# Performance work log

Measured on AMD Instinct MI355X. Metric: run time of the kernel, lower is better.

The kernel has to match this reference:

```python
import jax, jax.numpy as jnp
import numpy as np
from jax import lax


def setup_inputs() -> dict:
    key = jax.random.key(0)
    ks = jax.random.split(key, 5)
    T, H, F, E = 2048, 1024, 2816, 8
    scale_h = 1.0 / np.sqrt(H)
    scale_f = 1.0 / np.sqrt(F)
    return {
        "x": jax.random.normal(ks[0], (T, H), dtype=jnp.float32),
        "router_w": jax.random.normal(ks[1], (H, E), dtype=jnp.float32) * scale_h,
        "w_gate": jax.random.normal(ks[2], (E, H, F), dtype=jnp.float32) * scale_h,
        "w_up": jax.random.normal(ks[3], (E, H, F), dtype=jnp.float32) * scale_h,
        "w_down": jax.random.normal(ks[4], (E, F, H), dtype=jnp.float32) * scale_f,
        "top_k": 2,
    }


def reference(x, router_w, w_gate, w_up, w_down, top_k):
    # x: [T, H] flat tokens; router_w: [H, E]; experts: SwiGLU FFN (silu(x Wg) * (x Wu)) Wd
    T = x.shape[0]
    E = router_w.shape[1]
    logits = x @ router_w                              # [T, E]
    probs = jax.nn.softmax(logits, axis=-1)            # router_use_softmax
    top_v, top_i = lax.top_k(probs, top_k)             # [T, K]
    top_v = top_v / jnp.sum(top_v, axis=-1, keepdims=True)  # normalize_topk_prob
    # dense combine weights [T, E], zero outside top-k (top-k indices are unique per row)
    comb = jnp.zeros((T, E), dtype=x.dtype).at[jnp.arange(T)[:, None], top_i].set(top_v)

    def expert_step(acc, args):
        wg, wu, wd, c = args                           # wg/wu: [H,F], wd: [F,H], c: [T]
        g = jnp.einsum("th,hf->tf", x, wg)
        u = jnp.einsum("th,hf->tf", x, wu)
        y = jnp.einsum("tf,fh->th", jax.nn.silu(g) * u, wd)
        return acc + c[:, None] * y, None

    out, _ = lax.scan(expert_step, jnp.zeros_like(x), (w_gate, w_up, w_down, comb.T))
    return out
```

## Files before the change

kernel.cpp:

```cpp
#include <hip/hip_runtime.h>
#include <hip/hip_bf16.h>
#include <cstdint>
#include <cstddef>

#define TT 2048
#define HH 1024
#define FF 2816
#define EE 8
#define BK 64
#define KT1 (HH / BK)
#define KT2 (FF / BK)
#define KS 4
#define KTPER (KT2 / KS)
#define NROWS (TT * 2)

typedef short bf16x8 __attribute__((ext_vector_type(8)));
typedef float f32x4v __attribute__((ext_vector_type(4)));
typedef float vf4    __attribute__((ext_vector_type(4)));
typedef unsigned int uint32;

typedef __attribute__((address_space(3))) unsigned int lds_u32;
typedef const __attribute__((address_space(1))) unsigned int glb_u32;

__device__ __forceinline__ void gll16(const void* g, unsigned char* l) {
    __builtin_amdgcn_global_load_lds((glb_u32*)g, (lds_u32*)l, 16, 0, 0);
}

__device__ __forceinline__ unsigned short f2bf(float f) {
    union { float f; uint32 u; } v; v.f = f;
    uint32 u = v.u;
    uint32 r = (u + 0x7FFFu + ((u >> 16) & 1u)) >> 16;
    return (unsigned short)r;
}

__device__ __forceinline__ void seg_of(const int* __restrict__ counts, int e,
                                       int& seg0, int& n_e) {
    int s = 0;
#pragma unroll
    for (int i = 0; i < EE; ++i) s += (i < e) ? counts[i] : 0;
    seg0 = s; n_e = counts[e];
}

__global__ void k_router(const float* __restrict__ x, const float* __restrict__ rw,
                         unsigned short* __restrict__ xb,
                         int* __restrict__ tke, float* __restrict__ tkw,
                         int* __restrict__ counts)
{
    int t = blockIdx.x * 4 + (threadIdx.x >> 6);
    int lane = threadIdx.x & 63;
    const float* xr = x + (size_t)t * HH;
    unsigned short* xbr = xb + (size_t)t * HH;
    float acc[EE];
#pragma unroll
    for (int e = 0; e < EE; ++e) acc[e] = 0.f;
#pragma unroll
    for (int i = 0; i < HH / 64; ++i) {
        int h = i * 64 + lane;
        float xv = xr[h];
        xbr[h] = f2bf(xv);
        const vf4* w = (const vf4*)(rw + (size_t)h * EE);
        vf4 w0 = w[0], w1 = w[1];
#pragma unroll
        for (int e = 0; e < 4; ++e) {
            acc[e]     = fmaf(xv, w0[e], acc[e]);
            acc[4 + e] = fmaf(xv, w1[e], acc[4 + e]);
        }
    }
#pragma unroll
    for (int e = 0; e < EE; ++e) {
        float v = acc[e];
#pragma unroll
        for (int m = 1; m < 64; m <<= 1) v += __shfl_xor(v, m, 64);
        acc[e] = v;
    }
    if (lane == 0) {
        int e1 = 0; float l1 = acc[0];
#pragma unroll
        for (int e = 1; e < EE; ++e) if (acc[e] > l1) { l1 = acc[e]; e1 = e; }
        int e2 = (e1 == 0) ? 1 : 0; float l2 = acc[e2];
#pragma unroll
        for (int e = 0; e < EE; ++e) if (e != e1 && acc[e] > l2) { l2 = acc[e]; e2 = e; }
        float w1 = 1.f / (1.f + __expf(l2 - l1));
        float w2 = 1.f - w1;
        tke[t * 2] = e1; tke[t * 2 + 1] = e2;
        tkw[t * 2] = w1; tkw[t * 2 + 1] = w2;
        atomicAdd(&counts[e1], 1);
        atomicAdd(&counts[e2], 1);
    }
}

__global__ __launch_bounds__(256)
void k_convert_w2(const float* __restrict__ wg, const float* __restrict__ wu,
                  unsigned short* __restrict__ wgT, unsigned short* __restrict__ wuT)
{
    const int z = blockIdx.z;
    const float* src = (z < EE) ? wg : wu;
    unsigned short* dst = (z < EE) ? wgT : wuT;
    const int e = z & (EE - 1);
    const int K = HH, N = FF;
    const int nb = blockIdx.x * 64, kb = blockIdx.y * 64;
    __shared__ unsigned short t_[64][68];
    const int tid = threadIdx.x;
    const float* s = src + ((size_t)e * K + kb) * N + nb;
    {
        int kk = tid >> 4, n4 = (tid & 15) * 4;
#pragma unroll
        for (int i = 0; i < 4; ++i) {
            int k = kk + i * 16;
            vf4 v = *(const vf4*)(s + (size_t)k * N + n4);
#pragma unroll
            for (int j = 0; j < 4; ++j) t_[n4 + j][k] = f2bf(v[j]);
        }
    }
    __syncthreads();
    {
        int n = tid >> 2, c = (tid & 3) * 16;
        unsigned short* d = dst + ((size_t)e * N + nb + n) * K + kb + c;
        uint4 u0 = *(const uint4*)&t_[n][c];
        uint4 u1 = *(const uint4*)&t_[n][c + 8];
        *(uint4*)(d) = u0;
        *(uint4*)(d + 8) = u1;
    }
}

__global__ __launch_bounds__(256)
void k_convert_wdT(const float* __restrict__ src, unsigned short* __restrict__ dst)
{
    const int e = blockIdx.z;
    const int K = FF, N = HH;
    const int nb = blockIdx.x * 64, kb = blockIdx.y * 64;
    __shared__ unsigned short t_[64][68];
    const int tid = threadIdx.x;
    const float* s = src + ((size_t)e * K + kb) * N + nb;
    {
        int kk = tid >> 4, n4 = (tid & 15) * 4;
#pragma unroll
        for (int i = 0; i < 4; ++i) {
            int k = kk + i * 16;
            vf4 v = *(const vf4*)(s + (size_t)k * N + n4);
#pragma unroll
            for (int j = 0; j < 4; ++j) t_[n4 + j][k] = f2bf(v[j]);
        }
    }
    __syncthreads();
    {
        int n = tid >> 2, c = (tid & 3) * 16;
        unsigned short* d = dst + ((size_t)e * N + nb + n) * K + kb + c;
        uint4 u0 = *(const uint4*)&t_[n][c];
        uint4 u1 = *(const uint4*)&t_[n][c + 8];
        *(uint4*)(d) = u0;
        *(uint4*)(d + 8) = u1;
    }
}

__global__ void k_scatter(const int* __restrict__ tke, const float* __restrict__ tkw,
                          const int* __restrict__ counts, int* __restrict__ cursor,
                          int* __restrict__ row_tok, int* __restrict__ row_slot,
                          float* __restrict__ row_w)
{
    int t = blockIdx.x * 256 + threadIdx.x;
    if (t >= TT) return;
    int pre[EE];
    {
        int s = 0;
#pragma unroll
        for (int i = 0; i < EE; ++i) { pre[i] = s; s += counts[i]; }
    }
#pragma unroll
    for (int k = 0; k < 2; ++k) {
        int e = tke[t * 2 + k];
        int pos = atomicAdd(&cursor[e], 1);
        int r = pre[e] + pos;
        row_tok[r] = t;
        row_slot[r] = k;
        row_w[r] = tkw[t * 2 + k];
    }
}

__global__ __launch_bounds__(256, 4)
void k_gemm1(const unsigned short* __restrict__ xb,
             const unsigned short* __restrict__ wgT, const unsigned short* __restrict__ wuT,
             const int* __restrict__ counts, const int* __restrict__ row_tok,
             unsigned short* __restrict__ hb)
{
    const int nbase = blockIdx.x * 64;
    const int e = blockIdx.y >> 4, mt = blockIdx.y & 15;
    int seg0, n_e; seg_of(counts, e, seg0, n_e);
    const int m0 = mt * 128;
    if (m0 >= n_e) return;

    __shared__ __align__(16) unsigned char smem[32768];
    const int tid = threadIdx.x, lane = tid & 63, wid = tid >> 6;
    const int wr = wid >> 1, wc = wid & 1;
    const int rl = lane >> 3, cbyte = (lane & 7) * 16;

    const char* a_src[4];
#pragma unroll
    for (int i = 0; i < 4; ++i) {
        int r = wid * 32 + i * 8 + rl;
        int gi = m0 + r; int cidx = gi < n_e ? gi : n_e - 1;
        int tok = row_tok[seg0 + cidx];
        a_src[i] = (const char*)xb + (size_t)tok * (HH * 2)
                 + (size_t)(cbyte ^ ((r & 7) << 4));
    }
    const char* bg_src[2]; const char* bu_src[2];
#pragma unroll
    for (int i = 0; i < 2; ++i) {
        int n = wid * 16 + i * 8 + rl;
        size_t rowoff = ((size_t)e * FF + nbase + n) * (HH * 2)
                      + (size_t)(cbyte ^ ((n & 7) << 4));
        bg_src[i] = (const char*)wgT + rowoff;
        bu_src[i] = (const char*)wuT + rowoff;
    }

    auto STAGE = [&](int kt) {
        size_t ko = (size_t)kt * 128;
#pragma unroll
        for (int i = 0; i < 4; ++i) gll16(a_src[i] + ko, smem + wid * 4096 + i * 1024);
#pragma unroll
        for (int i = 0; i < 2; ++i) gll16(bg_src[i] + ko, smem + 16384 + wid * 2048 + i * 1024);
#pragma unroll
        for (int i = 0; i < 2; ++i) gll16(bu_src[i] + ko, smem + 24576 + wid * 2048 + i * 1024);
    };

    f32x4v zero4 = {0.f, 0.f, 0.f, 0.f};
    f32x4v accg[4][2], accu[4][2];
#pragma unroll
    for (int mi = 0; mi < 4; ++mi)
#pragma unroll
        for (int ni = 0; ni < 2; ++ni) { accg[mi][ni] = zero4; accu[mi][ni] = zero4; }

    for (int kt = 0; kt < KT1; ++kt) {
        STAGE(kt);
        __syncthreads();
#pragma unroll
        for (int kk = 0; kk < 2; ++kk) {
            const int cb = kk * 64 + ((lane >> 4) << 4);
            bf16x8 af[4], bgf[2], buf_[2];
#pragma unroll
            for (int mi = 0; mi < 4; ++mi) {
                int r = wr * 64 + mi * 16 + (lane & 15);
                af[mi] = *(const bf16x8*)(smem + r * 128 + (cb ^ ((r & 7) << 4)));
            }
#pragma unroll
            for (int ni = 0; ni < 2; ++ni) {
                int n = wc * 32 + ni * 16 + (lane & 15);
                int off = n * 128 + (cb ^ ((n & 7) << 4));
                bgf[ni]  = *(const bf16x8*)(smem + 16384 + off);
                buf_[ni] = *(const bf16x8*)(smem + 24576 + off);
            }
#pragma unroll
            for (int mi = 0; mi < 4; ++mi)
#pragma unroll
                for (int ni = 0; ni < 2; ++ni) {
                    accg[mi][ni] = __builtin_amdgcn_mfma_f32_16x16x32_bf16(af[mi], bgf[ni],  accg[mi][ni], 0, 0, 0);
                    accu[mi][ni] = __builtin_amdgcn_mfma_f32_16x16x32_bf16(af[mi], buf_[ni], accu[mi][ni], 0, 0, 0);
                }
        }
        __syncthreads();
    }

    const int lr = lane >> 4, lc = lane & 15;
#pragma unroll
    for (int mi = 0; mi < 4; ++mi) {
#pragma unroll
        for (int reg = 0; reg < 4; ++reg) {
            int r = wr * 64 + mi * 16 + lr * 4 + reg;
            int gi = m0 + r;
            if (gi < n_e) {
                size_t base = (size_t)(seg0 + gi) * FF;
#pragma unroll
                for (int ni = 0; ni < 2; ++ni) {
                    float g = accg[mi][ni][reg];
                    float u = accu[mi][ni][reg];
                    float hv = g * u / (1.f + __expf(-g));
                    int col = nbase + wc * 32 + ni * 16 + lc;
                    hb[base + col] = f2bf(hv);
                }
            }
        }
    }
}

__global__ __launch_bounds__(256, 4)
void k_gemm2(const unsigned short* __restrict__ hb, const unsigned short* __restrict__ wdT,
             const int* __restrict__ counts, const int* __restrict__ row_tok,
             const int* __restrict__ row_slot, const float* __restrict__ row_w,
             float* __restrict__ opart)
{
    const int nbase = blockIdx.x * 128;
    const int e = blockIdx.y >> 4, mt = blockIdx.y & 15;
    const int ks = blockIdx.z;
    int seg0, n_e; seg_of(counts, e, seg0, n_e);
    const int m0 = mt * 128;
    if (m0 >= n_e) return;
    const int kt0 = ks * KTPER;

    __shared__ __align__(16) unsigned char smem[32768];
    const int tid = threadIdx.x, lane = tid & 63, wid = tid >> 6;
    const int wr = wid >> 1, wc = wid & 1;
    const int rl = lane >> 3, cbyte = (lane & 7) * 16;

    const char* a_src[4];
#pragma unroll
    for (int i = 0; i < 4; ++i) {
        int r = wid * 32 + i * 8 + rl;
        int gi = m0 + r; int cidx = gi < n_e ? gi : n_e - 1;
        a_src[i] = (const char*)hb + (size_t)(seg0 + cidx) * (FF * 2)
                 + (size_t)(cbyte ^ ((r & 7) << 4));
    }
    const char* b_src[4];
#pragma unroll
    for (int i = 0; i < 4; ++i) {
        int n = wid * 32 + i * 8 + rl;
        b_src[i] = (const char*)wdT + ((size_t)e * HH + nbase + n) * (FF * 2)
                 + (size_t)(cbyte ^ ((n & 7) << 4));
    }

    auto STAGE = [&](int kt) {
        size_t ko = (size_t)kt * 128;
#pragma unroll
        for (int i = 0; i < 4; ++i) gll16(a_src[i] + ko, smem + wid * 4096 + i * 1024);
#pragma unroll
        for (int i = 0; i < 4; ++i) gll16(b_src[i] + ko, smem + 16384 + wid * 4096 + i * 1024);
    };

    f32x4v zero4 = {0.f, 0.f, 0.f, 0.f};
    f32x4v acc[4][4];
#pragma unroll
    for (int mi = 0; mi < 4; ++mi)
#pragma unroll
        for (int ni = 0; ni < 4; ++ni) acc[mi][ni] = zero4;

    for (int it = 0; it < KTPER; ++it) {
        STAGE(kt0 + it);
        __syncthreads();
#pragma unroll
        for (int kk = 0; kk < 2; ++kk) {
            const int cb = kk * 64 + ((lane >> 4) << 4);
            bf16x8 af[4], bf_[4];
#pragma unroll
            for (int mi = 0; mi < 4; ++mi) {
                int r = wr * 64 + mi * 16 + (lane & 15);
                af[mi] = *(const bf16x8*)(smem + r * 128 + (cb ^ ((r & 7) << 4)));
            }
#pragma unroll
            for (int ni = 0; ni < 4; ++ni) {
                int n = wc * 64 + ni * 16 + (lane & 15);
                bf_[ni] = *(const bf16x8*)(smem + 16384 + n * 128 + (cb ^ ((n & 7) << 4)));
            }
#pragma unroll
            for (int mi = 0; mi < 4; ++mi)
#pragma unroll
                for (int ni = 0; ni < 4; ++ni)
                    acc[mi][ni] = __builtin_amdgcn_mfma_f32_16x16x32_bf16(af[mi], bf_[ni], acc[mi][ni], 0, 0, 0);
        }
        __syncthreads();
    }

    const int lr = lane >> 4, lc = lane & 15;
#pragma unroll
    for (int mi = 0; mi < 4; ++mi) {
#pragma unroll
        for (int reg = 0; reg < 4; ++reg) {
            int r = wr * 64 + mi * 16 + lr * 4 + reg;
            int gi = m0 + r;
            if (gi < n_e) {
                int ar  = seg0 + gi;
                int tok = row_tok[ar];
                int sl  = row_slot[ar];
                float wgt = row_w[ar];
                size_t base = ((size_t)(ks * 2 + sl) * TT + tok) * HH;
#pragma unroll
                for (int ni = 0; ni < 4; ++ni) {
                    int col = nbase + wc * 64 + ni * 16 + lc;
                    opart[base + col] = wgt * acc[mi][ni][reg];
                }
            }
        }
    }
}

__global__ void k_combine(const float* __restrict__ opart, float* __restrict__ out)
{
    int i = (blockIdx.x * 256 + threadIdx.x) * 4;
    vf4 s = {0.f, 0.f, 0.f, 0.f};
#pragma unroll
    for (int k = 0; k < KS * 2; ++k)
        s += *(const vf4*)(opart + (size_t)k * TT * HH + i);
    *(vf4*)(out + i) = s;
}

extern "C" void kernel_launch(void* const* d_in, const int* in_sizes, int n_in,
                              void* d_out, int out_size, void* d_ws, size_t ws_size,
                              hipStream_t stream)
{
    (void)in_sizes; (void)n_in; (void)out_size; (void)ws_size;
    const float* x  = (const float*)d_in[0];
    const float* rw = (const float*)d_in[1];
    const float* wg = (const float*)d_in[2];
    const float* wu = (const float*)d_in[3];
    const float* wd = (const float*)d_in[4];
    float* out = (float*)d_out;

    char* ws = (char*)d_ws;
    size_t off = 0;
    auto alloc = [&](size_t b) { size_t o = off; off += (b + 255) & ~(size_t)255; return o; };
    unsigned short* xb  = (unsigned short*)(ws + alloc((size_t)TT * HH * 2));
    unsigned short* wgT = (unsigned short*)(ws + alloc((size_t)EE * FF * HH * 2));
    unsigned short* wuT = (unsigned short*)(ws + alloc((size_t)EE * FF * HH * 2));
    unsigned short* wdT = (unsigned short*)(ws + alloc((size_t)EE * HH * FF * 2));
    int*   tke      = (int*)  (ws + alloc((size_t)TT * 2 * 4));
    float* tkw      = (float*)(ws + alloc((size_t)TT * 2 * 4));
    int*   cc       = (int*)  (ws + alloc(2 * EE * 4));
    int*   counts   = cc;
    int*   cursor   = cc + EE;
    int*   row_tok  = (int*)  (ws + alloc((size_t)NROWS * 4));
    int*   row_slot = (int*)  (ws + alloc((size_t)NROWS * 4));
    float* row_w    = (float*)(ws + alloc((size_t)NROWS * 4));
    unsigned short* hb = (unsigned short*)(ws + alloc((size_t)NROWS * FF * 2));
    float* opart = (float*)wgT;

    hipMemsetAsync(cc, 0, 2 * EE * 4, stream);

    k_router<<<TT / 4, 256, 0, stream>>>(x, rw, xb, tke, tkw, counts);
    {
        dim3 gw(FF / 64, HH / 64, 2 * EE);
        k_convert_w2<<<gw, 256, 0, stream>>>(wg, wu, wgT, wuT);
        dim3 gd(HH / 64, FF / 64, EE);
        k_convert_wdT<<<gd, 256, 0, stream>>>(wd, wdT);
    }
    k_scatter<<<(TT + 255) / 256, 256, 0, stream>>>(tke, tkw, counts, cursor,
                                                    row_tok, row_slot, row_w);
    dim3 g1(FF / 64, 16 * EE);
    k_gemm1<<<g1, 256, 0, stream>>>(xb, wgT, wuT, counts, row_tok, hb);
    dim3 g2(HH / 128, 16 * EE, KS);
    k_gemm2<<<g2, 256, 0, stream>>>(hb, wdT, counts, row_tok, row_slot, row_w, opart);
    k_combine<<<(TT * HH) / (256 * 4), 256, 0, stream>>>(opart, out);
}
```

Before: 283.5 us.

## Enlarge weight-conversion transpose tiles to 128x128 with batched loads and packed LDS writes

The fp32-to-bf16 transpose kernels for the expert weights now process 128x128 tiles. Each thread issues 16 vector loads up front, packs pairs of bf16 values into 8-byte LDS writes, and writes 128-byte contiguous output rows. This is meant to raise memory-level parallelism and store efficiency in a bandwidth-bound preprocessing step. The weight conversions are also launched before the router. The padded LDS row stride of 138 elements leaves some vector LDS accesses not naturally aligned, which may cost extra LDS cycles.

```diff
diff --git a/kernel.cpp b/kernel.cpp
--- a/kernel.cpp
+++ b/kernel.cpp
@@ -98,28 +98,39 @@
     unsigned short* dst = (z < EE) ? wgT : wuT;
     const int e = z & (EE - 1);
     const int K = HH, N = FF;
-    const int nb = blockIdx.x * 64, kb = blockIdx.y * 64;
-    __shared__ unsigned short t_[64][68];
+    const int nb = blockIdx.x * 128, kb = blockIdx.y * 128;
+    __shared__ unsigned short t_[128][138];
     const int tid = threadIdx.x;
-    const float* s = src + ((size_t)e * K + kb) * N + nb;
-    {
-        int kk = tid >> 4, n4 = (tid & 15) * 4;
-#pragma unroll
-        for (int i = 0; i < 4; ++i) {
-            int k = kk + i * 16;
-            vf4 v = *(const vf4*)(s + (size_t)k * N + n4);
-#pragma unroll
-            for (int j = 0; j < 4; ++j) t_[n4 + j][k] = f2bf(v[j]);
+    const int n0  = (tid & 31) * 4;
+    const int kq0 = (tid >> 5) * 4;
+    const float* s = src + ((size_t)e * K + kb) * N + nb + n0;
+    vf4 v[4][4];
+#pragma unroll
+    for (int b = 0; b < 4; ++b) {
+        const float* sb = s + (size_t)(kq0 + b * 32) * N;
+#pragma unroll
+        for (int r = 0; r < 4; ++r)
+            v[b][r] = *(const vf4*)(sb + (size_t)r * N);
+    }
+#pragma unroll
+    for (int b = 0; b < 4; ++b) {
+        int k0 = kq0 + b * 32;
+#pragma unroll
+        for (int j = 0; j < 4; ++j) {
+            uint2 o;
+            o.x = (uint32)f2bf(v[b][0][j]) | ((uint32)f2bf(v[b][1][j]) << 16);
+            o.y = (uint32)f2bf(v[b][2][j]) | ((uint32)f2bf(v[b][3][j]) << 16);
+            *(uint2*)&t_[n0 + j][k0] = o;
         }
     }
     __syncthreads();
     {
-        int n = tid >> 2, c = (tid & 3) * 16;
-        unsigned short* d = dst + ((size_t)e * N + nb + n) * K + kb + c;
-        uint4 u0 = *(const uint4*)&t_[n][c];
-        uint4 u1 = *(const uint4*)&t_[n][c + 8];
-        *(uint4*)(d) = u0;
-        *(uint4*)(d + 8) = u1;
+        const int row = tid >> 1, c = (tid & 1) * 64;
+        unsigned short* d = dst + ((size_t)e * N + nb + row) * K + kb + c;
+        const unsigned short* ls = &t_[row][c];
+#pragma unroll
+        for (int q = 0; q < 8; ++q)
+            *(uint4*)(d + q * 8) = *(const uint4*)(ls + q * 8);
     }
 }
 
@@ -128,28 +139,39 @@
 {
     const int e = blockIdx.z;
     const int K = FF, N = HH;
-    const int nb = blockIdx.x * 64, kb = blockIdx.y * 64;
-    __shared__ unsigned short t_[64][68];
+    const int nb = blockIdx.x * 128, kb = blockIdx.y * 128;
+    __shared__ unsigned short t_[128][138];
     const int tid = threadIdx.x;
-    const float* s = src + ((size_t)e * K + kb) * N + nb;
-    {
-        int kk = tid >> 4, n4 = (tid & 15) * 4;
-#pragma unroll
-        for (int i = 0; i < 4; ++i) {
-            int k = kk + i * 16;
-            vf4 v = *(const vf4*)(s + (size_t)k * N + n4);
-#pragma unroll
-            for (int j = 0; j < 4; ++j) t_[n4 + j][k] = f2bf(v[j]);
+    const int n0  = (tid & 31) * 4;
+    const int kq0 = (tid >> 5) * 4;
+    const float* s = src + ((size_t)e * K + kb) * N + nb + n0;
+    vf4 v[4][4];
+#pragma unroll
+    for (int b = 0; b < 4; ++b) {
+        const float* sb = s + (size_t)(kq0 + b * 32) * N;
+#pragma unroll
+        for (int r = 0; r < 4; ++r)
+            v[b][r] = *(const vf4*)(sb + (size_t)r * N);
+    }
+#pragma unroll
+    for (int b = 0; b < 4; ++b) {
+        int k0 = kq0 + b * 32;
+#pragma unroll
+        for (int j = 0; j < 4; ++j) {
+            uint2 o;
+            o.x = (uint32)f2bf(v[b][0][j]) | ((uint32)f2bf(v[b][1][j]) << 16);
+            o.y = (uint32)f2bf(v[b][2][j]) | ((uint32)f2bf(v[b][3][j]) << 16);
+            *(uint2*)&t_[n0 + j][k0] = o;
         }
     }
     __syncthreads();
     {
-        int n = tid >> 2, c = (tid & 3) * 16;
-        unsigned short* d = dst + ((size_t)e * N + nb + n) * K + kb + c;
-        uint4 u0 = *(const uint4*)&t_[n][c];
-        uint4 u1 = *(const uint4*)&t_[n][c + 8];
-        *(uint4*)(d) = u0;
-        *(uint4*)(d + 8) = u1;
+        const int row = tid >> 1, c = (tid & 1) * 64;
+        unsigned short* d = dst + ((size_t)e * N + nb + row) * K + kb + c;
+        const unsigned short* ls = &t_[row][c];
+#pragma unroll
+        for (int q = 0; q < 8; ++q)
+            *(uint4*)(d + q * 8) = *(const uint4*)(ls + q * 8);
     }
 }
 
@@ -423,13 +445,13 @@
 
     hipMemsetAsync(cc, 0, 2 * EE * 4, stream);
 
+    {
+        dim3 gd(HH / 128, FF / 128, EE);
+        k_convert_wdT<<<gd, 256, 0, stream>>>(wd, wdT);
+        dim3 gw(FF / 128, HH / 128, 2 * EE);
+        k_convert_w2<<<gw, 256, 0, stream>>>(wg, wu, wgT, wuT);
+    }
     k_router<<<TT / 4, 256, 0, stream>>>(x, rw, xb, tke, tkw, counts);
-    {
-        dim3 gw(FF / 64, HH / 64, 2 * EE);
-        k_convert_w2<<<gw, 256, 0, stream>>>(wg, wu, wgT, wuT);
-        dim3 gd(HH / 64, FF / 64, EE);
-        k_convert_wdT<<<gd, 256, 0, stream>>>(wd, wdT);
-    }
     k_scatter<<<(TT + 255) / 256, 256, 0, stream>>>(tke, tkw, counts, cursor,
                                                     row_tok, row_slot, row_w);
     dim3 g1(FF / 64, 16 * EE);
```

Measured after the change: 293.8 us. 3.6% more time.

## Fuse fp32-to-bf16 weight conversion into expert GEMM tile loads

Applied to the files above, without the earlier changes.

Drops the two standalone kernels that transposed and converted all expert weights to bf16 before the GEMMs. Each GEMM now loads fp32 weight tiles straight from global memory into registers, packs them to bf16 with v_cvt_pk_bf16_f32, and writes them transposed into swizzled LDS. This removes a full pass that reads and writes every expert weight. In exchange, fp32 weights are re-read by every active M-tile, and the B operand loses its asynchronous global_load_lds path, so load latency is less hidden. The partial-output buffer now gets its own workspace allocation instead of reusing the converted-weight buffer.

```diff
diff --git a/kernel.cpp b/kernel.cpp
--- a/kernel.cpp
+++ b/kernel.cpp
@@ -33,6 +33,12 @@
     return (unsigned short)r;
 }
 
+__device__ __forceinline__ uint32 cvtpk(float a, float b) {
+    uint32 r;
+    asm("v_cvt_pk_bf16_f32 %0, %1, %2" : "=v"(r) : "v"(a), "v"(b));
+    return r;
+}
+
 __device__ __forceinline__ void seg_of(const int* __restrict__ counts, int e,
                                        int& seg0, int& n_e) {
     int s = 0;
@@ -89,70 +95,6 @@
     }
 }
 
-__global__ __launch_bounds__(256)
-void k_convert_w2(const float* __restrict__ wg, const float* __restrict__ wu,
-                  unsigned short* __restrict__ wgT, unsigned short* __restrict__ wuT)
-{
-    const int z = blockIdx.z;
-    const float* src = (z < EE) ? wg : wu;
-    unsigned short* dst = (z < EE) ? wgT : wuT;
-    const int e = z & (EE - 1);
-    const int K = HH, N = FF;
-    const int nb = blockIdx.x * 64, kb = blockIdx.y * 64;
-    __shared__ unsigned short t_[64][68];
-    const int tid = threadIdx.x;
-    const float* s = src + ((size_t)e * K + kb) * N + nb;
-    {
-        int kk = tid >> 4, n4 = (tid & 15) * 4;
-#pragma unroll
-        for (int i = 0; i < 4; ++i) {
-            int k = kk + i * 16;
-            vf4 v = *(const vf4*)(s + (size_t)k * N + n4);
-#pragma unroll
-            for (int j = 0; j < 4; ++j) t_[n4 + j][k] = f2bf(v[j]);
-        }
-    }
-    __syncthreads();
-    {
-        int n = tid >> 2, c = (tid & 3) * 16;
-        unsigned short* d = dst + ((size_t)e * N + nb + n) * K + kb + c;
-        uint4 u0 = *(const uint4*)&t_[n][c];
-        uint4 u1 = *(const uint4*)&t_[n][c + 8];
-        *(uint4*)(d) = u0;
-        *(uint4*)(d + 8) = u1;
-    }
-}
-
-__global__ __launch_bounds__(256)
-void k_convert_wdT(const float* __restrict__ src, unsigned short* __restrict__ dst)
-{
-    const int e = blockIdx.z;
-    const int K = FF, N = HH;
-    const int nb = blockIdx.x * 64, kb = blockIdx.y * 64;
-    __shared__ unsigned short t_[64][68];
-    const int tid = threadIdx.x;
-    const float* s = src + ((size_t)e * K + kb) * N + nb;
-    {
-        int kk = tid >> 4, n4 = (tid & 15) * 4;
-#pragma unroll
-        for (int i = 0; i < 4; ++i) {
-            int k = kk + i * 16;
-            vf4 v = *(const vf4*)(s + (size_t)k * N + n4);
-#pragma unroll
-            for (int j = 0; j < 4; ++j) t_[n4 + j][k] = f2bf(v[j]);
-        }
-    }
-    __syncthreads();
-    {
-        int n = tid >> 2, c = (tid & 3) * 16;
-        unsigned short* d = dst + ((size_t)e * N + nb + n) * K + kb + c;
-        uint4 u0 = *(const uint4*)&t_[n][c];
-        uint4 u1 = *(const uint4*)&t_[n][c + 8];
-        *(uint4*)(d) = u0;
-        *(uint4*)(d + 8) = u1;
-    }
-}
-
 __global__ void k_scatter(const int* __restrict__ tke, const float* __restrict__ tkw,
                           const int* __restrict__ counts, int* __restrict__ cursor,
                           int* __restrict__ row_tok, int* __restrict__ row_slot,
@@ -179,7 +121,7 @@
 
 __global__ __launch_bounds__(256, 4)
 void k_gemm1(const unsigned short* __restrict__ xb,
-             const unsigned short* __restrict__ wgT, const unsigned short* __restrict__ wuT,
+             const float* __restrict__ wg, const float* __restrict__ wu,
              const int* __restrict__ counts, const int* __restrict__ row_tok,
              unsigned short* __restrict__ hb)
 {
@@ -203,25 +145,15 @@
         a_src[i] = (const char*)xb + (size_t)tok * (HH * 2)
                  + (size_t)(cbyte ^ ((r & 7) << 4));
     }
-    const char* bg_src[2]; const char* bu_src[2];
-#pragma unroll
-    for (int i = 0; i < 2; ++i) {
-        int n = wid * 16 + i * 8 + rl;
-        size_t rowoff = ((size_t)e * FF + nbase + n) * (HH * 2)
-                      + (size_t)(cbyte ^ ((n & 7) << 4));
-        bg_src[i] = (const char*)wgT + rowoff;
-        bu_src[i] = (const char*)wuT + rowoff;
-    }
-
-    auto STAGE = [&](int kt) {
-        size_t ko = (size_t)kt * 128;
-#pragma unroll
-        for (int i = 0; i < 4; ++i) gll16(a_src[i] + ko, smem + wid * 4096 + i * 1024);
-#pragma unroll
-        for (int i = 0; i < 2; ++i) gll16(bg_src[i] + ko, smem + 16384 + wid * 2048 + i * 1024);
-#pragma unroll
-        for (int i = 0; i < 2; ++i) gll16(bu_src[i] + ko, smem + 24576 + wid * 2048 + i * 1024);
-    };
+    const int bn0 = (tid & 15) * 4, bk0 = (tid >> 4) * 4;
+    int b_lds[4];
+#pragma unroll
+    for (int j = 0; j < 4; ++j) {
+        int n = bn0 + j;
+        b_lds[j] = n * 128 + ((bk0 * 2) ^ ((n & 7) << 4));
+    }
+    const float* bgbase = wg + (size_t)e * HH * FF + nbase + bn0;
+    const float* bubase = wu + (size_t)e * HH * FF + nbase + bn0;
 
     f32x4v zero4 = {0.f, 0.f, 0.f, 0.f};
     f32x4v accg[4][2], accu[4][2];
@@ -231,7 +163,26 @@
         for (int ni = 0; ni < 2; ++ni) { accg[mi][ni] = zero4; accu[mi][ni] = zero4; }
 
     for (int kt = 0; kt < KT1; ++kt) {
-        STAGE(kt);
+        vf4 vg[4], vu[4];
+#pragma unroll
+        for (int r = 0; r < 4; ++r) {
+            size_t ro = (size_t)(kt * BK + bk0 + r) * FF;
+            vg[r] = *(const vf4*)(bgbase + ro);
+            vu[r] = *(const vf4*)(bubase + ro);
+        }
+        {
+            size_t ko = (size_t)kt * 128;
+#pragma unroll
+            for (int i = 0; i < 4; ++i) gll16(a_src[i] + ko, smem + wid * 4096 + i * 1024);
+        }
+#pragma unroll
+        for (int j = 0; j < 4; ++j) {
+            uint2 og, ou;
+            og.x = cvtpk(vg[0][j], vg[1][j]); og.y = cvtpk(vg[2][j], vg[3][j]);
+            ou.x = cvtpk(vu[0][j], vu[1][j]); ou.y = cvtpk(vu[2][j], vu[3][j]);
+            *(uint2*)(smem + 16384 + b_lds[j]) = og;
+            *(uint2*)(smem + 24576 + b_lds[j]) = ou;
+        }
         __syncthreads();
 #pragma unroll
         for (int kk = 0; kk < 2; ++kk) {
@@ -283,7 +234,7 @@
 }
 
 __global__ __launch_bounds__(256, 4)
-void k_gemm2(const unsigned short* __restrict__ hb, const unsigned short* __restrict__ wdT,
+void k_gemm2(const unsigned short* __restrict__ hb, const float* __restrict__ wd,
              const int* __restrict__ counts, const int* __restrict__ row_tok,
              const int* __restrict__ row_slot, const float* __restrict__ row_w,
              float* __restrict__ opart)
@@ -309,21 +260,14 @@
         a_src[i] = (const char*)hb + (size_t)(seg0 + cidx) * (FF * 2)
                  + (size_t)(cbyte ^ ((r & 7) << 4));
     }
-    const char* b_src[4];
-#pragma unroll
-    for (int i = 0; i < 4; ++i) {
-        int n = wid * 32 + i * 8 + rl;
-        b_src[i] = (const char*)wdT + ((size_t)e * HH + nbase + n) * (FF * 2)
-                 + (size_t)(cbyte ^ ((n & 7) << 4));
-    }
-
-    auto STAGE = [&](int kt) {
-        size_t ko = (size_t)kt * 128;
-#pragma unroll
-        for (int i = 0; i < 4; ++i) gll16(a_src[i] + ko, smem + wid * 4096 + i * 1024);
-#pragma unroll
-        for (int i = 0; i < 4; ++i) gll16(b_src[i] + ko, smem + 16384 + wid * 4096 + i * 1024);
-    };
+    const int bn0 = (tid & 15) * 8, bk0 = (tid >> 4) * 4;
+    int b_lds[8];
+#pragma unroll
+    for (int j = 0; j < 8; ++j) {
+        int n = bn0 + j;
+        b_lds[j] = n * 128 + ((bk0 * 2) ^ ((n & 7) << 4));
+    }
+    const float* bbase = wd + (size_t)e * FF * HH + nbase + bn0;
 
     f32x4v zero4 = {0.f, 0.f, 0.f, 0.f};
     f32x4v acc[4][4];
@@ -333,7 +277,27 @@
         for (int ni = 0; ni < 4; ++ni) acc[mi][ni] = zero4;
 
     for (int it = 0; it < KTPER; ++it) {
-        STAGE(kt0 + it);
+        const int kt = kt0 + it;
+        vf4 v0[4], v1[4];
+#pragma unroll
+        for (int r = 0; r < 4; ++r) {
+            const float* rp = bbase + (size_t)(kt * BK + bk0 + r) * HH;
+            v0[r] = *(const vf4*)(rp);
+            v1[r] = *(const vf4*)(rp + 4);
+        }
+        {
+            size_t ko = (size_t)kt * 128;
+#pragma unroll
+            for (int i = 0; i < 4; ++i) gll16(a_src[i] + ko, smem + wid * 4096 + i * 1024);
+        }
+#pragma unroll
+        for (int j = 0; j < 4; ++j) {
+            uint2 oa, ob;
+            oa.x = cvtpk(v0[0][j], v0[1][j]); oa.y = cvtpk(v0[2][j], v0[3][j]);
+            ob.x = cvtpk(v1[0][j], v1[1][j]); ob.y = cvtpk(v1[2][j], v1[3][j]);
+            *(uint2*)(smem + 16384 + b_lds[j])     = oa;
+            *(uint2*)(smem + 16384 + b_lds[4 + j]) = ob;
+        }
         __syncthreads();
 #pragma unroll
         for (int kk = 0; kk < 2; ++kk) {
@@ -406,10 +370,7 @@
     char* ws = (char*)d_ws;
     size_t off = 0;
     auto alloc = [&](size_t b) { size_t o = off; off += (b + 255) & ~(size_t)255; return o; };
-    unsigned short* xb  = (unsigned short*)(ws + alloc((size_t)TT * HH * 2));
-    unsigned short* wgT = (unsigned short*)(ws + alloc((size_t)EE * FF * HH * 2));
-    unsigned short* wuT = (unsigned short*)(ws + alloc((size_t)EE * FF * HH * 2));
-    unsigned short* wdT = (unsigned short*)(ws + alloc((size_t)EE * HH * FF * 2));
+    unsigned short* xb = (unsigned short*)(ws + alloc((size_t)TT * HH * 2));
     int*   tke      = (int*)  (ws + alloc((size_t)TT * 2 * 4));
     float* tkw      = (float*)(ws + alloc((size_t)TT * 2 * 4));
     int*   cc       = (int*)  (ws + alloc(2 * EE * 4));
@@ -419,22 +380,16 @@
     int*   row_slot = (int*)  (ws + alloc((size_t)NROWS * 4));
     float* row_w    = (float*)(ws + alloc((size_t)NROWS * 4));
     unsigned short* hb = (unsigned short*)(ws + alloc((size_t)NROWS * FF * 2));
-    float* opart = (float*)wgT;
+    float* opart    = (float*)(ws + alloc((size_t)KS * 2 * TT * HH * 4));
 
     hipMemsetAsync(cc, 0, 2 * EE * 4, stream);
 
     k_router<<<TT / 4, 256, 0, stream>>>(x, rw, xb, tke, tkw, counts);
-    {
-        dim3 gw(FF / 64, HH / 64, 2 * EE);
-        k_convert_w2<<<gw, 256, 0, stream>>>(wg, wu, wgT, wuT);
-        dim3 gd(HH / 64, FF / 64, EE);
-        k_convert_wdT<<<gd, 256, 0, stream>>>(wd, wdT);
-    }
     k_scatter<<<(TT + 255) / 256, 256, 0, stream>>>(tke, tkw, counts, cursor,
                                                     row_tok, row_slot, row_w);
     dim3 g1(FF / 64, 16 * EE);
-    k_gemm1<<<g1, 256, 0, stream>>>(xb, wgT, wuT, counts, row_tok, hb);
+    k_gemm1<<<g1, 256, 0, stream>>>(xb, wg, wu, counts, row_tok, hb);
     dim3 g2(HH / 128, 16 * EE, KS);
-    k_gemm2<<<g2, 256, 0, stream>>>(hb, wdT, counts, row_tok, row_slot, row_w, opart);
+    k_gemm2<<<g2, 256, 0, stream>>>(hb, wd, counts, row_tok, row_slot, row_w, opart);
     k_combine<<<(TT * HH) / (256 * 4), 256, 0, stream>>>(opart, out);
 }
```

Result: slower. 334.5 us (+18.0%).
